# Optimization experiments

Measured on AMD Instinct MI355X. Metric: run time of the kernel, lower is better.

Reference implementation:

```python
import jax, jax.numpy as jnp
import numpy as np

B, D, A, H, NH = 32768, 768, 17, 128, 4
DH = H // NH


def _ln(x, g, b, eps=1e-5):
    mu = jnp.mean(x, axis=-1, keepdims=True)
    var = jnp.mean((x - mu) ** 2, axis=-1, keepdims=True)
    return (x - mu) / jnp.sqrt(var + eps) * g + b


def setup_inputs() -> dict:
    key = jax.random.key(0)
    ks = jax.random.split(key, 16)
    s = 0.02
    return {
        "visual_feat": jax.random.normal(ks[0], (B, D), jnp.float32),
        "au_feat": jax.random.uniform(ks[1], (B, A), jnp.float32),
        "w_tok": jax.random.normal(ks[2], (H, 1), jnp.float32) * s,
        "b_tok": jnp.zeros((H,), jnp.float32),
        "pos": jax.random.normal(ks[3], (1, A, H), jnp.float32) * s,
        "g_auln": jnp.ones((H,), jnp.float32),
        "b_auln": jnp.zeros((H,), jnp.float32),
        "w_q": jax.random.normal(ks[4], (H, D), jnp.float32) * s,
        "b_q": jnp.zeros((H,), jnp.float32),
        "w_in": jax.random.normal(ks[5], (3 * H, H), jnp.float32) * s,  # packed q,k,v in_proj
        "b_in": jnp.zeros((3 * H,), jnp.float32),
        "w_ao": jax.random.normal(ks[6], (H, H), jnp.float32) * s,  # MHA out_proj
        "b_ao": jnp.zeros((H,), jnp.float32),
        "g_aln": jnp.ones((H,), jnp.float32),
        "b_aln": jnp.zeros((H,), jnp.float32),
        "w_out": jax.random.normal(ks[7], (D, H), jnp.float32) * s,
        "b_out": jnp.zeros((D,), jnp.float32),
        "w_gate": jax.random.normal(ks[8], (D, 2 * D), jnp.float32) * s,
        "b_gate": jnp.zeros((D,), jnp.float32),
    }


def reference(visual_feat, au_feat, w_tok, b_tok, pos, g_auln, b_auln,
              w_q, b_q, w_in, b_in, w_ao, b_ao, g_aln, b_aln,
              w_out, b_out, w_gate, b_gate):
    # AU tokens: Linear(1 -> H) on intensities, + pos embed, LN. [B, A, H]
    au_tokens = au_feat[..., None] * w_tok[:, 0] + b_tok
    au_tokens = _ln(au_tokens + pos, g_auln, b_auln)
    # query: [B, H] (seq len 1)
    query = visual_feat @ w_q.T + b_q
    # MultiheadAttention (batch_first, packed in_proj)
    wq, wk, wv = w_in[:H], w_in[H:2 * H], w_in[2 * H:]
    bq, bk, bv = b_in[:H], b_in[H:2 * H], b_in[2 * H:]
    q = (query @ wq.T + bq).reshape(-1, NH, DH)          # [B, nh, dh]
    k = (au_tokens @ wk.T + bk).reshape(-1, A, NH, DH)   # [B, A, nh, dh]
    v = (au_tokens @ wv.T + bv).reshape(-1, A, NH, DH)
    scale = 1.0 / jnp.sqrt(jnp.asarray(DH, q.dtype))
    scores = jnp.einsum('bhd,bahd->bha', q * scale, k)   # [B, nh, A]
    attn = jax.nn.softmax(scores, axis=-1)
    ctx = jnp.einsum('bha,bahd->bhd', attn, v).reshape(-1, H)
    attn_out = ctx @ w_ao.T + b_ao
    attn_out = _ln(attn_out, g_aln, b_aln)
    attn_feat = attn_out @ w_out.T + b_out               # [B, D]
    gate_in = jnp.concatenate([visual_feat, attn_feat], axis=1)
    gate = jax.nn.sigmoid(gate_in @ w_gate.T + b_gate)
    return gate * attn_feat + (1.0 - gate) * visual_feat
```

## Files before the change

kernel.cpp:

```cpp
#include <hip/hip_runtime.h>
#include <hip/hip_bf16.h>

typedef __hip_bfloat16 bf16;
typedef __attribute__((ext_vector_type(8))) short short8;
typedef __attribute__((ext_vector_type(4))) float f32x4;
typedef __attribute__((ext_vector_type(8))) __bf16 bf16x8;
typedef const __attribute__((address_space(1))) void* gas_ptr;
typedef __attribute__((address_space(3))) void* las_ptr;

#define NB 32768
#define DD 768
#define AA 17
#define HH 128

__device__ __forceinline__ float bs2f(short s){
  unsigned int u = ((unsigned int)(unsigned short)s) << 16;
  return __builtin_bit_cast(float, u);
}
__device__ __forceinline__ short f2bs(float f){
  bf16 h = __float2bfloat16(f);
  return __builtin_bit_cast(short, h);
}
__device__ __forceinline__ f32x4 mfma16(short8 a, short8 b, f32x4 c){
  return __builtin_amdgcn_mfma_f32_16x16x32_bf16(
      __builtin_bit_cast(bf16x8, a), __builtin_bit_cast(bf16x8, b), c, 0, 0, 0);
}
__device__ __forceinline__ void glds16(const short* g, short* l){
  __builtin_amdgcn_global_load_lds((gas_ptr)g, (las_ptr)l, 16, 0, 0);
}

template<int F32>
__device__ __forceinline__ short8 ldchunk(const void* base, long elem_off){
  if (F32){
    const float4* p = (const float4*)((const float*)base + elem_off);
    float4 x = p[0], y = p[1];
    short8 r;
    r[0]=f2bs(x.x); r[1]=f2bs(x.y); r[2]=f2bs(x.z); r[3]=f2bs(x.w);
    r[4]=f2bs(y.x); r[5]=f2bs(y.y); r[6]=f2bs(y.z); r[7]=f2bs(y.w);
    return r;
  } else {
    return *(const short8*)((const short*)base + elem_off);
  }
}


__device__ __forceinline__ float blk_mean128(float v, float* tmp){
  int t = threadIdx.x;
  #pragma unroll
  for (int m = 32; m; m >>= 1) v += __shfl_xor(v, m);
  if ((t & 63) == 0) tmp[t >> 6] = v;
  __syncthreads();
  float r = (tmp[0] + tmp[1]) * (1.0f / 128.0f);
  __syncthreads();
  return r;
}

__global__ void prep1(const float* __restrict__ w_tok, const float* __restrict__ b_tok,
                      const float* __restrict__ pos, const float* __restrict__ g_auln,
                      float* __restrict__ ug, float* __restrict__ rg, float* __restrict__ coef){
  __shared__ float tmp[2];
  int h = threadIdx.x;
  float w = w_tok[h];
  float wbar = blk_mean128(w, tmp);
  float u = w - wbar;
  float g = g_auln[h];
  ug[h] = u * g;
  float muu = blk_mean128(u * u, tmp);
  if (h == 0) coef[0] = muu;
  float bt = b_tok[h];
  for (int a = 0; a < AA; ++a){
    float c = bt + pos[a * HH + h];
    float cbar = blk_mean128(c, tmp);
    float r = c - cbar;
    rg[a * HH + h] = r * g;
    float mur = blk_mean128(u * r, tmp);
    float mrr = blk_mean128(r * r, tmp);
    if (h == 0){ coef[1 + a] = mur; coef[18 + a] = mrr; }
  }
}

__global__ void prep2(const float* __restrict__ w_in, const float* __restrict__ b_in,
                      const float* __restrict__ b_auln, const float* __restrict__ b_q,
                      const float* __restrict__ ug, const float* __restrict__ rg,
                      float* __restrict__ Uk, float* __restrict__ Ck,
                      float* __restrict__ Uv, float* __restrict__ Cv,
                      float* __restrict__ Rk, float* __restrict__ Rv,
                      float* __restrict__ bqf){
  int hp = threadIdx.x, bid = blockIdx.x;
  const float* wqrow = w_in + (long)hp * HH;
  const float* wkrow = w_in + (long)(HH + hp) * HH;
  const float* wvrow = w_in + (long)(2 * HH + hp) * HH;
  if (bid < AA){
    int a = bid;
    float sk = 0.f, sv = 0.f;
    for (int t = 0; t < HH; ++t){
      float r = rg[a * HH + t];
      sk += r * wkrow[t];
      sv += r * wvrow[t];
    }
    Rk[a * HH + hp] = sk; Rv[a * HH + hp] = sv;
  } else if (bid == AA){
    float uk = 0.f, uv = 0.f, ck = 0.f, cv = 0.f;
    for (int t = 0; t < HH; ++t){
      float u = ug[t], ba = b_auln[t];
      float wk = wkrow[t], wv = wvrow[t];
      uk += u * wk; uv += u * wv; ck += ba * wk; cv += ba * wv;
    }
    Uk[hp] = uk; Uv[hp] = uv;
    Ck[hp] = ck + b_in[HH + hp];
    Cv[hp] = cv + b_in[2 * HH + hp];
  } else {
    float s = 0.f;
    for (int t = 0; t < HH; ++t) s += b_q[t] * wqrow[t];
    bqf[hp] = s + b_in[hp];
  }
}

__global__ void prep_wqf(const float* __restrict__ w_in, const float* __restrict__ w_q,
                         bf16* __restrict__ Wqf){
  __shared__ float wq[HH];
  int h = blockIdx.x, t = threadIdx.x;
  if (t < HH) wq[t] = w_in[(long)h * HH + t];
  __syncthreads();
  for (int j = t; j < DD; j += 256){
    float acc = 0.f;
    for (int k = 0; k < HH; ++k) acc += wq[k] * w_q[(long)k * DD + j];
    Wqf[(long)h * DD + j] = __float2bfloat16(acc);
  }
}

__global__ void prep_gate(const float* __restrict__ w_gate, const float* __restrict__ b_gate,
                          const float* __restrict__ w_out, const float* __restrict__ b_out,
                          bf16* __restrict__ Wg1b, bf16* __restrict__ Wg2w,
                          bf16* __restrict__ Woutb, float* __restrict__ bgp){
  __shared__ float wg2[DD];
  __shared__ float red[2];
  int c = blockIdx.x, t = threadIdx.x;
  const float* wrow = w_gate + (long)c * (2 * DD);
  for (int j = t; j < DD; j += 128){
    Wg1b[(long)c * DD + j] = __float2bfloat16(wrow[j]);
    wg2[j] = wrow[DD + j];
  }
  __syncthreads();
  float acc = 0.f;
  for (int j = 0; j < DD; ++j) acc = fmaf(wg2[j], w_out[(long)j * HH + t], acc);
  Wg2w[(long)c * HH + t] = __float2bfloat16(acc);
  Woutb[(long)c * HH + t] = __float2bfloat16(w_out[(long)c * HH + t]);
  float pb = 0.f;
  for (int j = t; j < DD; j += 128) pb = fmaf(wg2[j], b_out[j], pb);
  #pragma unroll
  for (int m = 32; m; m >>= 1) pb += __shfl_xor(pb, m);
  if ((t & 63) == 0) red[t >> 6] = pb;
  __syncthreads();
  if (t == 0) bgp[c] = b_gate[c] + red[0] + red[1];
}

__global__ __launch_bounds__(128) void attn(
    const bf16* __restrict__ Q, const float* __restrict__ au, const float* __restrict__ coef,
    const float* __restrict__ Uk_, const float* __restrict__ Ck_,
    const float* __restrict__ Uv_, const float* __restrict__ Cv_,
    const float* __restrict__ Rk, const float* __restrict__ Rv,
    bf16* __restrict__ ctx){
  const int ROWS = 8;
  int h = threadIdx.x;
  long row0 = (long)blockIdx.x * ROWS;
  float Uk = Uk_[h], Ck = Ck_[h], Uv = Uv_[h], Cv = Cv_[h];
  float cA = coef[0];
  __shared__ float sa[ROWS * AA];
  for (int idx = h; idx < ROWS * AA; idx += 128)
    sa[idx] = au[row0 * AA + idx];
  __syncthreads();
  const float scale = 0.17677669529663689f;
  for (int r = 0; r < ROWS; ++r){
    long row = row0 + r;
    float q = __bfloat162float(Q[row * HH + h]);
    float sc[AA], vv[AA];
    #pragma unroll
    for (int a = 0; a < AA; ++a){
      float s = sa[r * AA + a];
      float var = fmaf(s * s, cA, fmaf(2.f * s, coef[1 + a], coef[18 + a]));
      float rinv = rsqrtf(fmaxf(var, 0.f) + 1e-5f);
      float kk = fmaf(s, Uk, Rk[a * HH + h]) * rinv + Ck;
      vv[a]    = fmaf(s, Uv, Rv[a * HH + h]) * rinv + Cv;
      float p = q * kk;
      p += __shfl_xor(p, 16); p += __shfl_xor(p, 8); p += __shfl_xor(p, 4);
      p += __shfl_xor(p, 2);  p += __shfl_xor(p, 1);
      sc[a] = p * scale;
    }
    float mx = sc[0];
    #pragma unroll
    for (int a = 1; a < AA; ++a) mx = fmaxf(mx, sc[a]);
    float den = 0.f, cval = 0.f;
    #pragma unroll
    for (int a = 0; a < AA; ++a){
      float e = __expf(sc[a] - mx);
      den += e; cval += e * vv[a];
    }
    ctx[row * HH + h] = __float2bfloat16(cval / den);
  }
}

template<int MODE, int AF, int BF, int SIDE>
__global__ __launch_bounds__(256) void gemm_bt(
    const void* __restrict__ A, long lda, int ks,
    const void* __restrict__ Bw, long ldb,
    const float* __restrict__ bias,
    const float* __restrict__ g_ln, const float* __restrict__ b_ln,
    short* __restrict__ sideA,
    bf16* __restrict__ C, long ldc)
{
  __shared__ __align__(16) short smem[20480];
  const int tid = threadIdx.x;
  const int w = tid >> 6, l = tid & 63;
  const long rowBase = (long)blockIdx.y * 128;
  const int colBase = blockIdx.x * 128;
  const int fr = l & 15;
  const int kq = l >> 4;
  const int sr0 = tid >> 2,         sp0 = (tid & 3) * 8;
  const int sr1 = (tid + 256) >> 2;

  f32x4 acc[2][8];
  f32x4 zero = {0.f, 0.f, 0.f, 0.f};
  #pragma unroll
  for (int i = 0; i < 2; ++i)
    #pragma unroll
    for (int j = 0; j < 8; ++j) acc[i][j] = zero;

  {
    short8 av0 = ldchunk<AF>(A, (rowBase + sr0) * lda + sp0);
    short8 av1 = ldchunk<AF>(A, (rowBase + sr1) * lda + sp0);
    short8 bv0 = ldchunk<BF>(Bw, (long)(colBase + sr0) * ldb + sp0);
    short8 bv1 = ldchunk<BF>(Bw, (long)(colBase + sr1) * ldb + sp0);
    if (SIDE){
      *(short8*)(sideA + (rowBase + sr0) * lda + sp0) = av0;
      *(short8*)(sideA + (rowBase + sr1) * lda + sp0) = av1;
    }
    *(short8*)(smem + sr0 * 40 + sp0) = av0;
    *(short8*)(smem + sr1 * 40 + sp0) = av1;
    *(short8*)(smem + 5120 + sr0 * 40 + sp0) = bv0;
    *(short8*)(smem + 5120 + sr1 * 40 + sp0) = bv1;
  }

  for (int kt = 0; kt < ks; ++kt){
    __syncthreads();
    short* cb = smem + (kt & 1) * 10240;
    short* nb = smem + ((kt + 1) & 1) * 10240;
    const bool pf = (kt + 1 < ks);
    short8 av0, av1, bv0, bv1;
    if (pf){
      const long kA = (long)(kt + 1) * 32;
      av0 = ldchunk<AF>(A, (rowBase + sr0) * lda + kA + sp0);
      av1 = ldchunk<AF>(A, (rowBase + sr1) * lda + kA + sp0);
      bv0 = ldchunk<BF>(Bw, (long)(colBase + sr0) * ldb + kA + sp0);
      bv1 = ldchunk<BF>(Bw, (long)(colBase + sr1) * ldb + kA + sp0);
      if (SIDE){
        *(short8*)(sideA + (rowBase + sr0) * lda + kA + sp0) = av0;
        *(short8*)(sideA + (rowBase + sr1) * lda + kA + sp0) = av1;
      }
    }
    const int ra0 = w * 32 + fr;
    short8 a0 = *(const short8*)(cb + ra0 * 40 + kq * 8);
    short8 a1 = *(const short8*)(cb + (ra0 + 16) * 40 + kq * 8);
    #pragma unroll
    for (int nt = 0; nt < 8; ++nt){
      short8 b = *(const short8*)(cb + 5120 + (nt * 16 + fr) * 40 + kq * 8);
      acc[0][nt] = mfma16(a0, b, acc[0][nt]);
      acc[1][nt] = mfma16(a1, b, acc[1][nt]);
    }
    if (pf){
      *(short8*)(nb + sr0 * 40 + sp0) = av0;
      *(short8*)(nb + sr1 * 40 + sp0) = av1;
      *(short8*)(nb + 5120 + sr0 * 40 + sp0) = bv0;
      *(short8*)(nb + 5120 + sr1 * 40 + sp0) = bv1;
    }
  }
  __syncthreads();

  short* ep = smem;
  if (MODE == 1){
    #pragma unroll
    for (int mt = 0; mt < 2; ++mt){
      #pragma unroll
      for (int r = 0; r < 4; ++r){
        float x[8]; float sm = 0.f, sq = 0.f;
        #pragma unroll
        for (int nt = 0; nt < 8; ++nt){
          const int col = colBase + nt * 16 + fr;
          x[nt] = acc[mt][nt][r] + bias[col];
          sm += x[nt]; sq += x[nt] * x[nt];
        }
        sm += __shfl_xor(sm, 1); sq += __shfl_xor(sq, 1);
        sm += __shfl_xor(sm, 2); sq += __shfl_xor(sq, 2);
        sm += __shfl_xor(sm, 4); sq += __shfl_xor(sq, 4);
        sm += __shfl_xor(sm, 8); sq += __shfl_xor(sq, 8);
        const float mu = sm * (1.f / 128.f);
        const float var = sq * (1.f / 128.f) - mu * mu;
        const float rinv = rsqrtf(fmaxf(var, 0.f) + 1e-5f);
        const int lrow = w * 32 + mt * 16 + kq * 4 + r;
        #pragma unroll
        for (int nt = 0; nt < 8; ++nt){
          const int col = colBase + nt * 16 + fr;
          float y = (x[nt] - mu) * rinv * g_ln[col] + b_ln[col];
          ep[lrow * 136 + nt * 16 + fr] = f2bs(y);
        }
      }
    }
  } else {
    #pragma unroll
    for (int nt = 0; nt < 8; ++nt){
      const int col = colBase + nt * 16 + fr;
      const float bv = bias[col];
      #pragma unroll
      for (int mt = 0; mt < 2; ++mt){
        const int lrow0 = w * 32 + mt * 16 + kq * 4;
        #pragma unroll
        for (int r = 0; r < 4; ++r)
          ep[(lrow0 + r) * 136 + nt * 16 + fr] = f2bs(acc[mt][nt][r] + bv);
      }
    }
  }
  __syncthreads();

  #pragma unroll
  for (int it = 0; it < 8; ++it){
    const int cid = tid + it * 256;
    const int rw = cid >> 4;
    const int cc = (cid & 15) * 8;
    const long gr = rowBase + rw;
    short8 vls = *(const short8*)(ep + rw * 136 + cc);
    short* cp = (short*)C + gr * ldc + colBase + cc;
    *(short8*)cp = vls;
  }
}

template<int A1F>
__global__ __launch_bounds__(256) void gemm_final(
    const void* __restrict__ A1,
    const bf16* __restrict__ aon,
    const bf16* __restrict__ Wg1b,
    const bf16* __restrict__ Wg2w,
    const bf16* __restrict__ Woutb,
    const float* __restrict__ bgp,
    const float* __restrict__ b_out,
    const float* __restrict__ vf,
    float* __restrict__ C)
{
  __shared__ __align__(16) short smem[16384];
  const int tid = threadIdx.x;
  const int wv = tid >> 6, l = tid & 63;

  const int nx = 6;
  const int bid = blockIdx.y * nx + blockIdx.x;
  const int cpx = (NB / 128) * nx / 8;
  const int swz = (bid & 7) * cpx + (bid >> 3);
  const long rowBase = (long)(swz / nx) * 128;
  const int colBase = (swz % nx) * 128;

  const int fr = l & 15;
  const int kq = l >> 4;
  const int swofs = ((kq ^ ((l >> 1) & 3)) << 3);

  f32x4 accG[2][8], accF[2][8];
  f32x4 zero = {0.f, 0.f, 0.f, 0.f};
  #pragma unroll
  for (int i = 0; i < 2; ++i)
    #pragma unroll
    for (int j = 0; j < 8; ++j){ accG[i][j] = zero; accF[i][j] = zero; }

  if (A1F == 0){
    const short* Ab = (const short*)A1;
    const short* Bb = (const short*)Wg1b;
    const int srow = l >> 2;
    const int schunk = ((l & 3) ^ ((l >> 3) & 3)) * 8;
    #define STAGE_P1(p, kt) {                                                        \
      short* dA = smem + (p) * 8192;                                                 \
      _Pragma("unroll")                                                              \
      for (int i = 0; i < 2; ++i){                                                   \
        const int r = wv * 32 + i * 16 + srow;                                       \
        glds16(Ab + ((rowBase + r) * (long)DD + (kt) * 32 + schunk),                 \
               dA + wv * 1024 + i * 512);                                            \
        glds16(Bb + ((long)(colBase + r) * DD + (kt) * 32 + schunk),                 \
               dA + 4096 + wv * 1024 + i * 512);                                     \
      }                                                                              \
    }
    STAGE_P1(0, 0);
    for (int kt = 0; kt < DD / 32; ++kt){
      __syncthreads();
      if (kt + 1 < DD / 32) STAGE_P1((kt + 1) & 1, kt + 1);
      short* cb = smem + (kt & 1) * 8192;
      const int ra0 = wv * 32 + fr;
      short8 a0 = *(const short8*)(cb + ra0 * 32 + swofs);
      short8 a1 = *(const short8*)(cb + (ra0 + 16) * 32 + swofs);
      #pragma unroll
      for (int nt = 0; nt < 8; ++nt){
        short8 b = *(const short8*)(cb + 4096 + (nt * 16 + fr) * 32 + swofs);
        accG[0][nt] = mfma16(a0, b, accG[0][nt]);
        accG[1][nt] = mfma16(a1, b, accG[1][nt]);
      }
    }
    #undef STAGE_P1
  } else {
    const int sr0 = tid >> 2, sc = tid & 3;
    const int sr1 = sr0 + 64;
    const int sp = sc * 8;
    const int ss0 = (sc ^ ((sr0 >> 1) & 3)) * 8;
    const int ss1 = (sc ^ ((sr1 >> 1) & 3)) * 8;
    for (int kt = 0; kt < DD / 32; ++kt){
      const long kA = (long)kt * 32;
      short8 av0 = ldchunk<1>(A1, (rowBase + sr0) * (long)DD + kA + sp);
      short8 av1 = ldchunk<1>(A1, (rowBase + sr1) * (long)DD + kA + sp);
      short8 bv0 = *(const short8*)((const short*)Wg1b + (long)(colBase + sr0) * DD + kA + sp);
      short8 bv1 = *(const short8*)((const short*)Wg1b + (long)(colBase + sr1) * DD + kA + sp);
      __syncthreads();
      *(short8*)(smem + sr0 * 32 + ss0) = av0;
      *(short8*)(smem + sr1 * 32 + ss1) = av1;
      *(short8*)(smem + 4096 + sr0 * 32 + ss0) = bv0;
      *(short8*)(smem + 4096 + sr1 * 32 + ss1) = bv1;
      __syncthreads();
      const int ra0 = wv * 32 + fr;
      short8 a0 = *(const short8*)(smem + ra0 * 32 + swofs);
      short8 a1 = *(const short8*)(smem + (ra0 + 16) * 32 + swofs);
      #pragma unroll
      for (int nt = 0; nt < 8; ++nt){
        short8 b = *(const short8*)(smem + 4096 + (nt * 16 + fr) * 32 + swofs);
        accG[0][nt] = mfma16(a0, b, accG[0][nt]);
        accG[1][nt] = mfma16(a1, b, accG[1][nt]);
      }
    }
  }

  {
    short* As = smem;
    short* Bs = smem + 5120;
    short* Bs2 = smem + 10240;
    const int sr0 = tid >> 2, sp0 = (tid & 3) * 8;
    const int sr1 = sr0 + 64;
    for (int kt = 0; kt < HH / 32; ++kt){
      const long kA = (long)kt * 32;
      short8 av0 = *(const short8*)((const short*)aon + (rowBase + sr0) * HH + kA + sp0);
      short8 av1 = *(const short8*)((const short*)aon + (rowBase + sr1) * HH + kA + sp0);
      short8 bv0 = *(const short8*)((const short*)Wg2w + (long)(colBase + sr0) * HH + kA + sp0);
      short8 bv1 = *(const short8*)((const short*)Wg2w + (long)(colBase + sr1) * HH + kA + sp0);
      short8 cv0 = *(const short8*)((const short*)Woutb + (long)(colBase + sr0) * HH + kA + sp0);
      short8 cv1 = *(const short8*)((const short*)Woutb + (long)(colBase + sr1) * HH + kA + sp0);
      __syncthreads();
      *(short8*)(As + sr0 * 40 + sp0) = av0;
      *(short8*)(As + sr1 * 40 + sp0) = av1;
      *(short8*)(Bs + sr0 * 40 + sp0) = bv0;
      *(short8*)(Bs + sr1 * 40 + sp0) = bv1;
      *(short8*)(Bs2 + sr0 * 40 + sp0) = cv0;
      *(short8*)(Bs2 + sr1 * 40 + sp0) = cv1;
      __syncthreads();
      const int ra0 = wv * 32 + fr;
      short8 a0 = *(const short8*)(As + ra0 * 40 + kq * 8);
      short8 a1 = *(const short8*)(As + (ra0 + 16) * 40 + kq * 8);
      #pragma unroll
      for (int nt = 0; nt < 8; ++nt){
        short8 b  = *(const short8*)(Bs  + (nt * 16 + fr) * 40 + kq * 8);
        short8 b2 = *(const short8*)(Bs2 + (nt * 16 + fr) * 40 + kq * 8);
        accG[0][nt] = mfma16(a0, b,  accG[0][nt]);
        accG[1][nt] = mfma16(a1, b,  accG[1][nt]);
        accF[0][nt] = mfma16(a0, b2, accF[0][nt]);
        accF[1][nt] = mfma16(a1, b2, accF[1][nt]);
      }
    }
  }

  float bg[8], bo[8];
  #pragma unroll
  for (int nt = 0; nt < 8; ++nt){
    const int col = colBase + nt * 16 + fr;
    bg[nt] = bgp[col];
    bo[nt] = b_out[col];
  }
  #pragma unroll
  for (int mt = 0; mt < 2; ++mt){
    const long r0 = rowBase + wv * 32 + mt * 16 + kq * 4;
    #pragma unroll
    for (int r = 0; r < 4; ++r){
      const long row = r0 + r;
      const float* vrow = vf + row * DD;
      float* crow = C + row * DD;
      #pragma unroll
      for (int nt = 0; nt < 8; ++nt){
        const int col = colBase + nt * 16 + fr;
        const float lin = accG[mt][nt][r] + bg[nt];
        const float afv = accF[mt][nt][r] + bo[nt];
        const float gate = 1.f / (1.f + __expf(-lin));
        crow[col] = gate * afv + (1.f - gate) * vrow[col];
      }
    }
  }
}

extern "C" void kernel_launch(void* const* d_in, const int* in_sizes, int n_in,
                              void* d_out, int out_size, void* d_ws, size_t ws_size,
                              hipStream_t stream){
  const float* visual = (const float*)d_in[0];
  const float* au     = (const float*)d_in[1];
  const float* w_tok  = (const float*)d_in[2];
  const float* b_tok  = (const float*)d_in[3];
  const float* pos    = (const float*)d_in[4];
  const float* g_auln = (const float*)d_in[5];
  const float* b_auln = (const float*)d_in[6];
  const float* w_q    = (const float*)d_in[7];
  const float* b_q    = (const float*)d_in[8];
  const float* w_in   = (const float*)d_in[9];
  const float* b_in   = (const float*)d_in[10];
  const float* w_ao   = (const float*)d_in[11];
  const float* b_ao   = (const float*)d_in[12];
  const float* g_aln  = (const float*)d_in[13];
  const float* b_aln  = (const float*)d_in[14];
  const float* w_out  = (const float*)d_in[15];
  const float* b_out  = (const float*)d_in[16];
  const float* w_gate = (const float*)d_in[17];
  const float* b_gate = (const float*)d_in[18];

  char* ob = (char*)d_out;
  bf16* Q   = (bf16*)(ob);
  bf16* ctx = (bf16*)(ob + ((size_t)8 << 20));
  char* p = ob + ((size_t)16 << 20);
  auto alloc = [&](size_t bytes){ char* r = p; p += (bytes + 255) & ~(size_t)255; return r; };
  bf16*  Wqf  = (bf16*) alloc((size_t)HH * DD * 2);
  float* bqf  = (float*)alloc(HH * 4);
  float* ug   = (float*)alloc(HH * 4);
  float* rg   = (float*)alloc(AA * HH * 4);
  float* coef = (float*)alloc(64 * 4);
  float* Uk   = (float*)alloc(HH * 4);
  float* Ck   = (float*)alloc(HH * 4);
  float* Uv   = (float*)alloc(HH * 4);
  float* Cv   = (float*)alloc(HH * 4);
  float* Rk   = (float*)alloc(AA * HH * 4);
  float* Rv   = (float*)alloc(AA * HH * 4);

  char* q = (char*)d_ws;
  auto walloc = [&](size_t bytes){ char* r = q; q += (bytes + 255) & ~(size_t)255; return r; };
  bf16*  aon   = (bf16*) walloc((size_t)NB * HH * 2);
  bf16*  Wg1b  = (bf16*) walloc((size_t)DD * DD * 2);
  bf16*  Wg2w  = (bf16*) walloc((size_t)DD * HH * 2);
  bf16*  Woutb = (bf16*) walloc((size_t)DD * HH * 2);
  float* bgp   = (float*)walloc(DD * 4);
  bf16*  vbf   = (bf16*) walloc((size_t)NB * DD * 2);
  const bool use_vbf = (size_t)(q - (char*)d_ws) <= ws_size;

  prep1<<<dim3(1), dim3(128), 0, stream>>>(w_tok, b_tok, pos, g_auln, ug, rg, coef);
  prep2<<<dim3(19), dim3(128), 0, stream>>>(w_in, b_in, b_auln, b_q, ug, rg, Uk, Ck, Uv, Cv, Rk, Rv, bqf);
  prep_wqf<<<dim3(128), dim3(256), 0, stream>>>(w_in, w_q, Wqf);
  prep_gate<<<dim3(DD), dim3(128), 0, stream>>>(w_gate, b_gate, w_out, b_out, Wg1b, Wg2w, Woutb, bgp);

  if (use_vbf)
    gemm_bt<0, 1, 0, 1><<<dim3(1, NB / 128), dim3(256), 0, stream>>>(
        visual, (long)DD, DD / 32, Wqf, (long)DD,
        bqf, nullptr, nullptr, (short*)vbf, Q, (long)HH);
  else
    gemm_bt<0, 1, 0, 0><<<dim3(1, NB / 128), dim3(256), 0, stream>>>(
        visual, (long)DD, DD / 32, Wqf, (long)DD,
        bqf, nullptr, nullptr, nullptr, Q, (long)HH);

  attn<<<dim3(NB / 8), dim3(128), 0, stream>>>(Q, au, coef, Uk, Ck, Uv, Cv, Rk, Rv, ctx);

  gemm_bt<1, 0, 1, 0><<<dim3(1, NB / 128), dim3(256), 0, stream>>>(
      ctx, (long)HH, HH / 32, w_ao, (long)HH,
      b_ao, g_aln, b_aln, nullptr, aon, (long)HH);

  if (use_vbf)
    gemm_final<0><<<dim3(DD / 128, NB / 128), dim3(256), 0, stream>>>(
        vbf, aon, Wg1b, Wg2w, Woutb, bgp, b_out, visual, (float*)d_out);
  else
    gemm_final<1><<<dim3(DD / 128, NB / 128), dim3(256), 0, stream>>>(
        visual, aon, Wg1b, Wg2w, Woutb, bgp, b_out, visual, (float*)d_out);
}
```

Measured before the change: 498.0 us.

## Retile N=128 GEMMs to 32-row blocks, narrow final GEMM tiles, hoist attn weights

The two N=128 GEMMs become a new 128-thread kernel with 32-row tiles, XOR-swizzled LDS, async global-to-LDS loads for the bf16 weight, and a one-stage register prefetch of A. The out-projection weight is pre-converted to bf16 in prep_gate so it can use that path. The final gated GEMM switches from 128x128 to 128x64 tiles (12 column tiles) with glds loads in the K=128 phase, and the attention kernel hoists per-head Rk/Rv loads out of the row loop. The aim is more blocks for occupancy and fewer redundant loads. The cost is that each visual row tile is now re-read by twice as many column blocks in the final GEMM.

```diff
diff --git a/kernel.cpp b/kernel.cpp
--- a/kernel.cpp
+++ b/kernel.cpp
@@ -13,10 +13,6 @@
 #define AA 17
 #define HH 128
 
-__device__ __forceinline__ float bs2f(short s){
-  unsigned int u = ((unsigned int)(unsigned short)s) << 16;
-  return __builtin_bit_cast(float, u);
-}
 __device__ __forceinline__ short f2bs(float f){
   bf16 h = __float2bfloat16(f);
   return __builtin_bit_cast(short, h);
@@ -131,8 +127,10 @@
 
 __global__ void prep_gate(const float* __restrict__ w_gate, const float* __restrict__ b_gate,
                           const float* __restrict__ w_out, const float* __restrict__ b_out,
+                          const float* __restrict__ w_ao,
                           bf16* __restrict__ Wg1b, bf16* __restrict__ Wg2w,
-                          bf16* __restrict__ Woutb, float* __restrict__ bgp){
+                          bf16* __restrict__ Woutb, float* __restrict__ bgp,
+                          bf16* __restrict__ w_ao_bf){
   __shared__ float wg2[DD];
   __shared__ float red[2];
   int c = blockIdx.x, t = threadIdx.x;
@@ -141,6 +139,7 @@
     Wg1b[(long)c * DD + j] = __float2bfloat16(wrow[j]);
     wg2[j] = wrow[DD + j];
   }
+  if (c < HH) w_ao_bf[(long)c * HH + t] = __float2bfloat16(w_ao[(long)c * HH + t]);
   __syncthreads();
   float acc = 0.f;
   for (int j = 0; j < DD; ++j) acc = fmaf(wg2[j], w_out[(long)j * HH + t], acc);
@@ -166,6 +165,12 @@
   long row0 = (long)blockIdx.x * ROWS;
   float Uk = Uk_[h], Ck = Ck_[h], Uv = Uv_[h], Cv = Cv_[h];
   float cA = coef[0];
+  float rk[AA], rv[AA];
+  #pragma unroll
+  for (int a = 0; a < AA; ++a){
+    rk[a] = Rk[a * HH + h];
+    rv[a] = Rv[a * HH + h];
+  }
   __shared__ float sa[ROWS * AA];
   for (int idx = h; idx < ROWS * AA; idx += 128)
     sa[idx] = au[row0 * AA + idx];
@@ -180,8 +185,8 @@
       float s = sa[r * AA + a];
       float var = fmaf(s * s, cA, fmaf(2.f * s, coef[1 + a], coef[18 + a]));
       float rinv = rsqrtf(fmaxf(var, 0.f) + 1e-5f);
-      float kk = fmaf(s, Uk, Rk[a * HH + h]) * rinv + Ck;
-      vv[a]    = fmaf(s, Uv, Rv[a * HH + h]) * rinv + Cv;
+      float kk = fmaf(s, Uk, rk[a]) * rinv + Ck;
+      vv[a]    = fmaf(s, Uv, rv[a]) * rinv + Cv;
       float p = q * kk;
       p += __shfl_xor(p, 16); p += __shfl_xor(p, 8); p += __shfl_xor(p, 4);
       p += __shfl_xor(p, 2);  p += __shfl_xor(p, 1);
@@ -200,78 +205,72 @@
   }
 }
 
-template<int MODE, int AF, int BF, int SIDE>
-__global__ __launch_bounds__(256) void gemm_bt(
+template<int MODE, int AF, int SIDE>
+__global__ __launch_bounds__(128) void gemm_n128(
     const void* __restrict__ A, long lda, int ks,
-    const void* __restrict__ Bw, long ldb,
+    const bf16* __restrict__ Bw, long ldb,
     const float* __restrict__ bias,
     const float* __restrict__ g_ln, const float* __restrict__ b_ln,
     short* __restrict__ sideA,
-    bf16* __restrict__ C, long ldc)
+    bf16* __restrict__ C)
 {
-  __shared__ __align__(16) short smem[20480];
+  __shared__ __align__(16) short smem[10240];
   const int tid = threadIdx.x;
-  const int w = tid >> 6, l = tid & 63;
-  const long rowBase = (long)blockIdx.y * 128;
-  const int colBase = blockIdx.x * 128;
-  const int fr = l & 15;
-  const int kq = l >> 4;
-  const int sr0 = tid >> 2,         sp0 = (tid & 3) * 8;
-  const int sr1 = (tid + 256) >> 2;
-
-  f32x4 acc[2][8];
+  const int wv = tid >> 6, l = tid & 63;
+  const long rowBase = (long)blockIdx.x * 32;
+  const int fr = l & 15, kq = l >> 4;
+  const int swofs = (kq ^ ((l >> 1) & 3)) << 3;
+  const int arow = tid >> 2, ac = tid & 3;
+  const int asl = (ac ^ ((arow >> 1) & 3)) * 8;
+  const int srow = l >> 2;
+  const int schunk = ((l & 3) ^ ((l >> 3) & 3)) * 8;
+
+  f32x4 acc[8];
   f32x4 zero = {0.f, 0.f, 0.f, 0.f};
   #pragma unroll
-  for (int i = 0; i < 2; ++i)
-    #pragma unroll
-    for (int j = 0; j < 8; ++j) acc[i][j] = zero;
-
+  for (int j = 0; j < 8; ++j) acc[j] = zero;
+
+  short8 avh;
   {
-    short8 av0 = ldchunk<AF>(A, (rowBase + sr0) * lda + sp0);
-    short8 av1 = ldchunk<AF>(A, (rowBase + sr1) * lda + sp0);
-    short8 bv0 = ldchunk<BF>(Bw, (long)(colBase + sr0) * ldb + sp0);
-    short8 bv1 = ldchunk<BF>(Bw, (long)(colBase + sr1) * ldb + sp0);
-    if (SIDE){
-      *(short8*)(sideA + (rowBase + sr0) * lda + sp0) = av0;
-      *(short8*)(sideA + (rowBase + sr1) * lda + sp0) = av1;
-    }
-    *(short8*)(smem + sr0 * 40 + sp0) = av0;
-    *(short8*)(smem + sr1 * 40 + sp0) = av1;
-    *(short8*)(smem + 5120 + sr0 * 40 + sp0) = bv0;
-    *(short8*)(smem + 5120 + sr1 * 40 + sp0) = bv1;
-  }
-
+    short8 av0 = ldchunk<AF>(A, (rowBase + arow) * lda + ac * 8);
+    if (SIDE) *(short8*)(sideA + (rowBase + arow) * lda + ac * 8) = av0;
+    *(short8*)(smem + arow * 32 + asl) = av0;
+    #pragma unroll
+    for (int i = 0; i < 4; ++i){
+      const int brow = wv * 64 + i * 16 + srow;
+      glds16((const short*)Bw + (long)brow * ldb + schunk,
+             smem + 1024 + wv * 2048 + i * 512);
+    }
+    if (ks > 1){
+      avh = ldchunk<AF>(A, (rowBase + arow) * lda + 32 + ac * 8);
+      if (SIDE) *(short8*)(sideA + (rowBase + arow) * lda + 32 + ac * 8) = avh;
+    }
+  }
   for (int kt = 0; kt < ks; ++kt){
     __syncthreads();
-    short* cb = smem + (kt & 1) * 10240;
-    short* nb = smem + ((kt + 1) & 1) * 10240;
-    const bool pf = (kt + 1 < ks);
-    short8 av0, av1, bv0, bv1;
-    if (pf){
-      const long kA = (long)(kt + 1) * 32;
-      av0 = ldchunk<AF>(A, (rowBase + sr0) * lda + kA + sp0);
-      av1 = ldchunk<AF>(A, (rowBase + sr1) * lda + kA + sp0);
-      bv0 = ldchunk<BF>(Bw, (long)(colBase + sr0) * ldb + kA + sp0);
-      bv1 = ldchunk<BF>(Bw, (long)(colBase + sr1) * ldb + kA + sp0);
-      if (SIDE){
-        *(short8*)(sideA + (rowBase + sr0) * lda + kA + sp0) = av0;
-        *(short8*)(sideA + (rowBase + sr1) * lda + kA + sp0) = av1;
-      }
-    }
-    const int ra0 = w * 32 + fr;
-    short8 a0 = *(const short8*)(cb + ra0 * 40 + kq * 8);
-    short8 a1 = *(const short8*)(cb + (ra0 + 16) * 40 + kq * 8);
+    short* cb = smem + (kt & 1) * 5120;
+    short* nb = smem + ((kt + 1) & 1) * 5120;
+    if (kt + 1 < ks){
+      *(short8*)(nb + arow * 32 + asl) = avh;
+      const long kB = (long)(kt + 1) * 32;
+      #pragma unroll
+      for (int i = 0; i < 4; ++i){
+        const int brow = wv * 64 + i * 16 + srow;
+        glds16((const short*)Bw + (long)brow * ldb + kB + schunk,
+               nb + 1024 + wv * 2048 + i * 512);
+      }
+      if (kt + 2 < ks){
+        const long kA = (long)(kt + 2) * 32;
+        avh = ldchunk<AF>(A, (rowBase + arow) * lda + kA + ac * 8);
+        if (SIDE) *(short8*)(sideA + (rowBase + arow) * lda + kA + ac * 8) = avh;
+      }
+    }
+    const int ra = wv * 16 + fr;
+    short8 a0 = *(const short8*)(cb + ra * 32 + swofs);
     #pragma unroll
     for (int nt = 0; nt < 8; ++nt){
-      short8 b = *(const short8*)(cb + 5120 + (nt * 16 + fr) * 40 + kq * 8);
-      acc[0][nt] = mfma16(a0, b, acc[0][nt]);
-      acc[1][nt] = mfma16(a1, b, acc[1][nt]);
-    }
-    if (pf){
-      *(short8*)(nb + sr0 * 40 + sp0) = av0;
-      *(short8*)(nb + sr1 * 40 + sp0) = av1;
-      *(short8*)(nb + 5120 + sr0 * 40 + sp0) = bv0;
-      *(short8*)(nb + 5120 + sr1 * 40 + sp0) = bv1;
+      short8 b = *(const short8*)(cb + 1024 + (nt * 16 + fr) * 32 + swofs);
+      acc[nt] = mfma16(a0, b, acc[nt]);
     }
   }
   __syncthreads();
@@ -279,57 +278,45 @@
   short* ep = smem;
   if (MODE == 1){
     #pragma unroll
-    for (int mt = 0; mt < 2; ++mt){
-      #pragma unroll
-      for (int r = 0; r < 4; ++r){
-        float x[8]; float sm = 0.f, sq = 0.f;
-        #pragma unroll
-        for (int nt = 0; nt < 8; ++nt){
-          const int col = colBase + nt * 16 + fr;
-          x[nt] = acc[mt][nt][r] + bias[col];
-          sm += x[nt]; sq += x[nt] * x[nt];
-        }
-        sm += __shfl_xor(sm, 1); sq += __shfl_xor(sq, 1);
-        sm += __shfl_xor(sm, 2); sq += __shfl_xor(sq, 2);
-        sm += __shfl_xor(sm, 4); sq += __shfl_xor(sq, 4);
-        sm += __shfl_xor(sm, 8); sq += __shfl_xor(sq, 8);
-        const float mu = sm * (1.f / 128.f);
-        const float var = sq * (1.f / 128.f) - mu * mu;
-        const float rinv = rsqrtf(fmaxf(var, 0.f) + 1e-5f);
-        const int lrow = w * 32 + mt * 16 + kq * 4 + r;
-        #pragma unroll
-        for (int nt = 0; nt < 8; ++nt){
-          const int col = colBase + nt * 16 + fr;
-          float y = (x[nt] - mu) * rinv * g_ln[col] + b_ln[col];
-          ep[lrow * 136 + nt * 16 + fr] = f2bs(y);
-        }
+    for (int r = 0; r < 4; ++r){
+      float x[8]; float sm = 0.f, sq = 0.f;
+      #pragma unroll
+      for (int nt = 0; nt < 8; ++nt){
+        x[nt] = acc[nt][r] + bias[nt * 16 + fr];
+        sm += x[nt]; sq += x[nt] * x[nt];
+      }
+      sm += __shfl_xor(sm, 1); sq += __shfl_xor(sq, 1);
+      sm += __shfl_xor(sm, 2); sq += __shfl_xor(sq, 2);
+      sm += __shfl_xor(sm, 4); sq += __shfl_xor(sq, 4);
+      sm += __shfl_xor(sm, 8); sq += __shfl_xor(sq, 8);
+      const float mu = sm * (1.f / 128.f);
+      const float var = sq * (1.f / 128.f) - mu * mu;
+      const float rinv = rsqrtf(fmaxf(var, 0.f) + 1e-5f);
+      const int lrow = wv * 16 + kq * 4 + r;
+      #pragma unroll
+      for (int nt = 0; nt < 8; ++nt){
+        const int col = nt * 16 + fr;
+        float y = (x[nt] - mu) * rinv * g_ln[col] + b_ln[col];
+        ep[lrow * 136 + col] = f2bs(y);
       }
     }
   } else {
     #pragma unroll
     for (int nt = 0; nt < 8; ++nt){
-      const int col = colBase + nt * 16 + fr;
-      const float bv = bias[col];
-      #pragma unroll
-      for (int mt = 0; mt < 2; ++mt){
-        const int lrow0 = w * 32 + mt * 16 + kq * 4;
-        #pragma unroll
-        for (int r = 0; r < 4; ++r)
-          ep[(lrow0 + r) * 136 + nt * 16 + fr] = f2bs(acc[mt][nt][r] + bv);
-      }
-    }
-  }
-  __syncthreads();
-
-  #pragma unroll
-  for (int it = 0; it < 8; ++it){
-    const int cid = tid + it * 256;
+      const float bv = bias[nt * 16 + fr];
+      #pragma unroll
+      for (int r = 0; r < 4; ++r)
+        ep[(wv * 16 + kq * 4 + r) * 136 + nt * 16 + fr] = f2bs(acc[nt][r] + bv);
+    }
+  }
+  __syncthreads();
+
+  #pragma unroll
+  for (int it = 0; it < 4; ++it){
+    const int cid = tid + it * 128;
     const int rw = cid >> 4;
     const int cc = (cid & 15) * 8;
-    const long gr = rowBase + rw;
-    short8 vls = *(const short8*)(ep + rw * 136 + cc);
-    short* cp = (short*)C + gr * ldc + colBase + cc;
-    *(short8*)cp = vls;
+    *(short8*)((short*)C + (rowBase + rw) * HH + cc) = *(const short8*)(ep + rw * 136 + cc);
   }
 }
 
@@ -345,83 +332,78 @@
     const float* __restrict__ vf,
     float* __restrict__ C)
 {
-  __shared__ __align__(16) short smem[16384];
+  __shared__ __align__(16) short smem[12288];
   const int tid = threadIdx.x;
   const int wv = tid >> 6, l = tid & 63;
 
-  const int nx = 6;
+  const int nx = 12;
   const int bid = blockIdx.y * nx + blockIdx.x;
   const int cpx = (NB / 128) * nx / 8;
   const int swz = (bid & 7) * cpx + (bid >> 3);
   const long rowBase = (long)(swz / nx) * 128;
-  const int colBase = (swz % nx) * 128;
+  const int colBase = (swz % nx) * 64;
 
   const int fr = l & 15;
   const int kq = l >> 4;
-  const int swofs = ((kq ^ ((l >> 1) & 3)) << 3);
-
-  f32x4 accG[2][8], accF[2][8];
+  const int swofs = (kq ^ ((l >> 1) & 3)) << 3;
+  const int srow = l >> 2;
+  const int schunk = ((l & 3) ^ ((l >> 3) & 3)) * 8;
+
+  f32x4 accG[2][4], accF[2][4];
   f32x4 zero = {0.f, 0.f, 0.f, 0.f};
   #pragma unroll
   for (int i = 0; i < 2; ++i)
     #pragma unroll
-    for (int j = 0; j < 8; ++j){ accG[i][j] = zero; accF[i][j] = zero; }
+    for (int j = 0; j < 4; ++j){ accG[i][j] = zero; accF[i][j] = zero; }
 
   if (A1F == 0){
     const short* Ab = (const short*)A1;
     const short* Bb = (const short*)Wg1b;
-    const int srow = l >> 2;
-    const int schunk = ((l & 3) ^ ((l >> 3) & 3)) * 8;
-    #define STAGE_P1(p, kt) {                                                        \
-      short* dA = smem + (p) * 8192;                                                 \
-      _Pragma("unroll")                                                              \
-      for (int i = 0; i < 2; ++i){                                                   \
-        const int r = wv * 32 + i * 16 + srow;                                       \
-        glds16(Ab + ((rowBase + r) * (long)DD + (kt) * 32 + schunk),                 \
-               dA + wv * 1024 + i * 512);                                            \
-        glds16(Bb + ((long)(colBase + r) * DD + (kt) * 32 + schunk),                 \
-               dA + 4096 + wv * 1024 + i * 512);                                     \
-      }                                                                              \
-    }
-    STAGE_P1(0, 0);
+    #define STAGE_F1(p, kt) {                                                 \
+      short* d = smem + (p) * 6144;                                           \
+      _Pragma("unroll")                                                       \
+      for (int i = 0; i < 2; ++i){                                            \
+        const int r = wv * 32 + i * 16 + srow;                                \
+        glds16(Ab + (rowBase + r) * (long)DD + (kt) * 32 + schunk,            \
+               d + wv * 1024 + i * 512);                                      \
+      }                                                                       \
+      glds16(Bb + (long)(colBase + wv * 16 + srow) * DD + (kt) * 32 + schunk, \
+             d + 4096 + wv * 512);                                            \
+    }
+    STAGE_F1(0, 0);
     for (int kt = 0; kt < DD / 32; ++kt){
       __syncthreads();
-      if (kt + 1 < DD / 32) STAGE_P1((kt + 1) & 1, kt + 1);
-      short* cb = smem + (kt & 1) * 8192;
+      if (kt + 1 < DD / 32) STAGE_F1((kt + 1) & 1, kt + 1);
+      short* cb = smem + (kt & 1) * 6144;
       const int ra0 = wv * 32 + fr;
       short8 a0 = *(const short8*)(cb + ra0 * 32 + swofs);
       short8 a1 = *(const short8*)(cb + (ra0 + 16) * 32 + swofs);
       #pragma unroll
-      for (int nt = 0; nt < 8; ++nt){
+      for (int nt = 0; nt < 4; ++nt){
         short8 b = *(const short8*)(cb + 4096 + (nt * 16 + fr) * 32 + swofs);
         accG[0][nt] = mfma16(a0, b, accG[0][nt]);
         accG[1][nt] = mfma16(a1, b, accG[1][nt]);
       }
     }
-    #undef STAGE_P1
+    #undef STAGE_F1
   } else {
-    const int sr0 = tid >> 2, sc = tid & 3;
-    const int sr1 = sr0 + 64;
-    const int sp = sc * 8;
-    const int ss0 = (sc ^ ((sr0 >> 1) & 3)) * 8;
-    const int ss1 = (sc ^ ((sr1 >> 1) & 3)) * 8;
+    const int r0 = tid >> 2, ac = tid & 3;
+    const int s0 = (ac ^ ((r0 >> 1) & 3)) * 8;
     for (int kt = 0; kt < DD / 32; ++kt){
       const long kA = (long)kt * 32;
-      short8 av0 = ldchunk<1>(A1, (rowBase + sr0) * (long)DD + kA + sp);
-      short8 av1 = ldchunk<1>(A1, (rowBase + sr1) * (long)DD + kA + sp);
-      short8 bv0 = *(const short8*)((const short*)Wg1b + (long)(colBase + sr0) * DD + kA + sp);
-      short8 bv1 = *(const short8*)((const short*)Wg1b + (long)(colBase + sr1) * DD + kA + sp);
+      short8 av0 = ldchunk<1>(A1, (rowBase + r0) * (long)DD + kA + ac * 8);
+      short8 av1 = ldchunk<1>(A1, (rowBase + 64 + r0) * (long)DD + kA + ac * 8);
+      short8 bv  = *(const short8*)((const short*)Wg1b + (long)(colBase + r0) * DD + kA + ac * 8);
       __syncthreads();
-      *(short8*)(smem + sr0 * 32 + ss0) = av0;
-      *(short8*)(smem + sr1 * 32 + ss1) = av1;
-      *(short8*)(smem + 4096 + sr0 * 32 + ss0) = bv0;
-      *(short8*)(smem + 4096 + sr1 * 32 + ss1) = bv1;
+      *(short8*)(smem + r0 * 32 + s0) = av0;
+      *(short8*)(smem + (64 + r0) * 32 + s0) = av1;
+      *(short8*)(smem + 4096 + r0 * 32 + s0) = bv;
       __syncthreads();
       const int ra0 = wv * 32 + fr;
       short8 a0 = *(const short8*)(smem + ra0 * 32 + swofs);
       short8 a1 = *(const short8*)(smem + (ra0 + 16) * 32 + swofs);
       #pragma unroll
-      for (int nt = 0; nt < 8; ++nt){
+      for (int nt = 0; nt < 4; ++nt){
         short8 b = *(const short8*)(smem + 4096 + (nt * 16 + fr) * 32 + swofs);
         accG[0][nt] = mfma16(a0, b, accG[0][nt]);
         accG[1][nt] = mfma16(a1, b, accG[1][nt]);
@@ -429,46 +411,37 @@
     }
   }
 
-  {
-    short* As = smem;
-    short* Bs = smem + 5120;
-    short* Bs2 = smem + 10240;
-    const int sr0 = tid >> 2, sp0 = (tid & 3) * 8;
-    const int sr1 = sr0 + 64;
-    for (int kt = 0; kt < HH / 32; ++kt){
-      const long kA = (long)kt * 32;
-      short8 av0 = *(const short8*)((const short*)aon + (rowBase + sr0) * HH + kA + sp0);
-      short8 av1 = *(const short8*)((const short*)aon + (rowBase + sr1) * HH + kA + sp0);
-      short8 bv0 = *(const short8*)((const short*)Wg2w + (long)(colBase + sr0) * HH + kA + sp0);
-      short8 bv1 = *(const short8*)((const short*)Wg2w + (long)(colBase + sr1) * HH + kA + sp0);
-      short8 cv0 = *(const short8*)((const short*)Woutb + (long)(colBase + sr0) * HH + kA + sp0);
-      short8 cv1 = *(const short8*)((const short*)Woutb + (long)(colBase + sr1) * HH + kA + sp0);
-      __syncthreads();
-      *(short8*)(As + sr0 * 40 + sp0) = av0;
-      *(short8*)(As + sr1 * 40 + sp0) = av1;
-      *(short8*)(Bs + sr0 * 40 + sp0) = bv0;
-      *(short8*)(Bs + sr1 * 40 + sp0) = bv1;
-      *(short8*)(Bs2 + sr0 * 40 + sp0) = cv0;
-      *(short8*)(Bs2 + sr1 * 40 + sp0) = cv1;
-      __syncthreads();
-      const int ra0 = wv * 32 + fr;
-      short8 a0 = *(const short8*)(As + ra0 * 40 + kq * 8);
-      short8 a1 = *(const short8*)(As + (ra0 + 16) * 40 + kq * 8);
-      #pragma unroll
-      for (int nt = 0; nt < 8; ++nt){
-        short8 b  = *(const short8*)(Bs  + (nt * 16 + fr) * 40 + kq * 8);
-        short8 b2 = *(const short8*)(Bs2 + (nt * 16 + fr) * 40 + kq * 8);
-        accG[0][nt] = mfma16(a0, b,  accG[0][nt]);
-        accG[1][nt] = mfma16(a1, b,  accG[1][nt]);
-        accF[0][nt] = mfma16(a0, b2, accF[0][nt]);
-        accF[1][nt] = mfma16(a1, b2, accF[1][nt]);
-      }
-    }
-  }
-
-  float bg[8], bo[8];
-  #pragma unroll
-  for (int nt = 0; nt < 8; ++nt){
+  for (int kt = 0; kt < HH / 32; ++kt){
+    __syncthreads();
+    const long kA = (long)kt * 32;
+    #pragma unroll
+    for (int i = 0; i < 2; ++i){
+      const int r = wv * 32 + i * 16 + srow;
+      glds16((const short*)aon + (rowBase + r) * HH + kA + schunk,
+             smem + wv * 1024 + i * 512);
+    }
+    glds16((const short*)Wg2w + (long)(colBase + wv * 16 + srow) * HH + kA + schunk,
+           smem + 4096 + wv * 512);
+    glds16((const short*)Woutb + (long)(colBase + wv * 16 + srow) * HH + kA + schunk,
+           smem + 6144 + wv * 512);
+    __syncthreads();
+    const int ra0 = wv * 32 + fr;
+    short8 a0 = *(const short8*)(smem + ra0 * 32 + swofs);
+    short8 a1 = *(const short8*)(smem + (ra0 + 16) * 32 + swofs);
+    #pragma unroll
+    for (int nt = 0; nt < 4; ++nt){
+      short8 b  = *(const short8*)(smem + 4096 + (nt * 16 + fr) * 32 + swofs);
+      short8 b2 = *(const short8*)(smem + 6144 + (nt * 16 + fr) * 32 + swofs);
+      accG[0][nt] = mfma16(a0, b,  accG[0][nt]);
+      accG[1][nt] = mfma16(a1, b,  accG[1][nt]);
+      accF[0][nt] = mfma16(a0, b2, accF[0][nt]);
+      accF[1][nt] = mfma16(a1, b2, accF[1][nt]);
+    }
+  }
+
+  float bg[4], bo[4];
+  #pragma unroll
+  for (int nt = 0; nt < 4; ++nt){
     const int col = colBase + nt * 16 + fr;
     bg[nt] = bgp[col];
     bo[nt] = b_out[col];
@@ -482,7 +455,7 @@
       const float* vrow = vf + row * DD;
       float* crow = C + row * DD;
       #pragma unroll
-      for (int nt = 0; nt < 8; ++nt){
+      for (int nt = 0; nt < 4; ++nt){
         const int col = colBase + nt * 16 + fr;
         const float lin = accG[mt][nt][r] + bg[nt];
         const float afv = accF[mt][nt][r] + bo[nt];
@@ -521,7 +494,8 @@
   bf16* ctx = (bf16*)(ob + ((size_t)8 << 20));
   char* p = ob + ((size_t)16 << 20);
   auto alloc = [&](size_t bytes){ char* r = p; p += (bytes + 255) & ~(size_t)255; return r; };
-  bf16*  Wqf  = (bf16*) alloc((size_t)HH * DD * 2);
+  bf16*  Wqf     = (bf16*) alloc((size_t)HH * DD * 2);
+  bf16*  w_ao_bf = (bf16*) alloc((size_t)HH * HH * 2);
   float* bqf  = (float*)alloc(HH * 4);
   float* ug   = (float*)alloc(HH * 4);
   float* rg   = (float*)alloc(AA * HH * 4);
@@ -546,27 +520,28 @@
   prep1<<<dim3(1), dim3(128), 0, stream>>>(w_tok, b_tok, pos, g_auln, ug, rg, coef);
   prep2<<<dim3(19), dim3(128), 0, stream>>>(w_in, b_in, b_auln, b_q, ug, rg, Uk, Ck, Uv, Cv, Rk, Rv, bqf);
   prep_wqf<<<dim3(128), dim3(256), 0, stream>>>(w_in, w_q, Wqf);
-  prep_gate<<<dim3(DD), dim3(128), 0, stream>>>(w_gate, b_gate, w_out, b_out, Wg1b, Wg2w, Woutb, bgp);
+  prep_gate<<<dim3(DD), dim3(128), 0, stream>>>(w_gate, b_gate, w_out, b_out, w_ao,
+                                                Wg1b, Wg2w, Woutb, bgp, w_ao_bf);
 
   if (use_vbf)
-    gemm_bt<0, 1, 0, 1><<<dim3(1, NB / 128), dim3(256), 0, stream>>>(
+    gemm_n128<0, 1, 1><<<dim3(NB / 32), dim3(128), 0, stream>>>(
         visual, (long)DD, DD / 32, Wqf, (long)DD,
-        bqf, nullptr, nullptr, (short*)vbf, Q, (long)HH);
+        bqf, nullptr, nullptr, (short*)vbf, Q);
   else
-    gemm_bt<0, 1, 0, 0><<<dim3(1, NB / 128), dim3(256), 0, stream>>>(
+    gemm_n128<0, 1, 0><<<dim3(NB / 32), dim3(128), 0, stream>>>(
         visual, (long)DD, DD / 32, Wqf, (long)DD,
-        bqf, nullptr, nullptr, nullptr, Q, (long)HH);
+        bqf, nullptr, nullptr, nullptr, Q);
 
   attn<<<dim3(NB / 8), dim3(128), 0, stream>>>(Q, au, coef, Uk, Ck, Uv, Cv, Rk, Rv, ctx);
 
-  gemm_bt<1, 0, 1, 0><<<dim3(1, NB / 128), dim3(256), 0, stream>>>(
-      ctx, (long)HH, HH / 32, w_ao, (long)HH,
-      b_ao, g_aln, b_aln, nullptr, aon, (long)HH);
+  gemm_n128<1, 0, 0><<<dim3(NB / 32), dim3(128), 0, stream>>>(
+      ctx, (long)HH, HH / 32, w_ao_bf, (long)HH,
+      b_ao, g_aln, b_aln, nullptr, aon);
 
   if (use_vbf)
-    gemm_final<0><<<dim3(DD / 128, NB / 128), dim3(256), 0, stream>>>(
+    gemm_final<0><<<dim3(12, NB / 128), dim3(256), 0, stream>>>(
         vbf, aon, Wg1b, Wg2w, Woutb, bgp, b_out, visual, (float*)d_out);
   else
-    gemm_final<1><<<dim3(DD / 128, NB / 128), dim3(256), 0, stream>>>(
+    gemm_final<1><<<dim3(12, NB / 128), dim3(256), 0, stream>>>(
         visual, aon, Wg1b, Wg2w, Woutb, bgp, b_out, visual, (float*)d_out);
 }
```

New measurement: 483.8 us. 1.03x faster.
